# Optimization experiments

Hardware: AMD Instinct MI355X
Metric: run time of the kernel (lower is better)

The kernel has to match this reference:

```python
import jax, jax.numpy as jnp
import numpy as np

B, S, D, H = 2, 2048, 2048, 16
DH = D // H  # 128


def setup_inputs() -> dict:
    key = jax.random.key(0)
    ks = jax.random.split(key, 7)
    x = jax.random.normal(ks[0], (B, S, D), dtype=jnp.float32)
    # causal mask [b, s, s], True = attend
    mask = jnp.broadcast_to(jnp.tril(jnp.ones((S, S), dtype=bool)), (B, S, S))
    scale = 1.0 / np.sqrt(D)
    Wq = jax.random.normal(ks[1], (D, H, DH), dtype=jnp.float32) * scale
    Wk = jax.random.normal(ks[2], (D, 1, DH), dtype=jnp.float32) * scale
    Wv = jax.random.normal(ks[3], (D, 1, DH), dtype=jnp.float32) * scale
    Wo = jax.random.normal(ks[4], (H, DH, D), dtype=jnp.float32) * scale
    bo = jnp.zeros((D,), dtype=jnp.float32)
    return {"x": x, "mask": mask, "Wq": Wq, "Wk": Wk, "Wv": Wv, "Wo": Wo, "bo": bo}


def reference(x, mask, Wq, Wk, Wv, Wo, bo):
    # projections: q [b,s,h,dh]; k,v [b,s,1,dh] (single shared KV head)
    q = jnp.einsum("bsd,dhe->bshe", x, Wq)
    k = jnp.einsum("bsd,dhe->bshe", x, Wk)[:, :, 0, :]  # [b,s,dh]
    v = jnp.einsum("bsd,dhe->bshe", x, Wv)[:, :, 0, :]  # [b,s,dh]
    # scores [b,h,s,s] with 1/sqrt(d_head) scaling
    scores = jnp.einsum("bqhe,bke->bhqk", q, k) / jnp.sqrt(
        jnp.asarray(q.shape[-1], dtype=q.dtype)
    )
    big_neg = jnp.finfo(scores.dtype).min
    scores = jnp.where(mask[:, None, :, :], scores, big_neg)
    probs = jax.nn.softmax(scores, axis=-1)
    attn = jnp.einsum("bhqk,bke->bhqe", probs, v)  # [b,h,s,dh]
    # output projection contracting (head, d_head) -> d_state, with bias
    out = jnp.einsum("bhqe,hed->bqd", attn, Wo) + bo
    return out
```

## Files before the change

kernel.cpp:

```cpp
#include <hip/hip_runtime.h>
#include <cmath>
#include <cstdint>

typedef __bf16 bf16;
typedef __bf16 bf16x8 __attribute__((ext_vector_type(8)));
typedef __bf16 bf16x4 __attribute__((ext_vector_type(4)));
typedef float f32x4 __attribute__((ext_vector_type(4)));

#define SDIM 2048
#define DDIM 2048
#define NQKV 2304
#define DH   128

__device__ __forceinline__ void glds16(const bf16* g, bf16* l) {
    __builtin_amdgcn_global_load_lds(
        (const __attribute__((address_space(1))) void*)g,
        (__attribute__((address_space(3))) void*)l, 16, 0, 0);
}

#define MEMFENCE() asm volatile("" ::: "memory")
#define SBAR() do { MEMFENCE(); __builtin_amdgcn_s_barrier(); MEMFENCE(); } while (0)

__global__ __launch_bounds__(256) void prep_kernel(const float* __restrict__ x,
                                                   const float* __restrict__ Wq,
                                                   const float* __restrict__ Wk,
                                                   const float* __restrict__ Wv,
                                                   const float* __restrict__ Wo,
                                                   bf16* __restrict__ xb,
                                                   bf16* __restrict__ Wqkv_t,
                                                   bf16* __restrict__ Wo_t) {
    __shared__ float tile[32][33];
    int bx = blockIdx.x;
    if (bx < 8192) {
        int i = bx * 256 + threadIdx.x;
        float4 v = reinterpret_cast<const float4*>(x)[i];
        bf16x4 o;
        o[0] = (bf16)v.x; o[1] = (bf16)v.y; o[2] = (bf16)v.z; o[3] = (bf16)v.w;
        reinterpret_cast<bf16x4*>(xb)[i] = o;
        return;
    }
    bx -= 8192;
    const float* src; bf16* dst; int srcN; int t;
    if (bx < 4096)      { src = Wq; dst = Wqkv_t;                      srcN = 2048; t = bx; }
    else if (bx < 4352) { src = Wk; dst = Wqkv_t + (size_t)2048*2048;  srcN = 128;  t = bx - 4096; }
    else if (bx < 4608) { src = Wv; dst = Wqkv_t + (size_t)2176*2048;  srcN = 128;  t = bx - 4352; }
    else                { src = Wo; dst = Wo_t;                        srcN = 2048; t = bx - 4608; }
    const int srcK = 2048;
    int ntx = srcN >> 5;
    int n0 = (t % ntx) * 32, k0 = (t / ntx) * 32;
    int tx = threadIdx.x & 31;
    int ty = threadIdx.x >> 5;
    for (int i = 0; i < 4; i++)
        tile[ty + i*8][tx] = src[(size_t)(k0 + ty + i*8) * srcN + n0 + tx];
    __syncthreads();
    for (int i = 0; i < 4; i++)
        dst[(size_t)(n0 + ty + i*8) * srcK + k0 + tx] = (bf16)tile[tx][ty + i*8];
}

template<int WRITE_F32, int BNW, int WRITE_VT>
__global__ __launch_bounds__(512, 2) void gemm9_kernel(const bf16* __restrict__ A,
                                                       const bf16* __restrict__ Bt,
                                                       void* __restrict__ Cout,
                                                       const float* __restrict__ bias,
                                                       bf16* __restrict__ Vt,
                                                       int N) {
    constexpr int K    = 2048;
    constexpr int NT   = 64;
    constexpr int ABUF = 8192;
    constexpr int BBUF = BNW * 2048;
    constexpr int GPT  = 2 + (BNW >> 1);
    __shared__ bf16 smem[3 * ABUF + 3 * BBUF];

    const int tid  = threadIdx.x;
    const int wave = tid >> 6, lane = tid & 63;
    const int quad = lane >> 4, l15 = lane & 15;
    const int wm = wave >> 2, wn = wave & 3;
    const int tm = blockIdx.x * 256, tn = blockIdx.y * (64 * BNW);

    const int rr = wave * 16 + (lane >> 2);
    const int cs = (lane & 3) ^ ((lane >> 3) & 3);
    const bf16* Ag = A  + (size_t)(tm + rr) * K + cs * 8;
    const bf16* Bg = Bt + (size_t)(tn + rr) * K + cs * 8;
    bf16* Asl = smem + wave * 512;
    bf16* Bsl = smem + 3 * ABUF + wave * 512;

    auto STAGE = [&](int t, int s3) {
        const bf16* sa = Ag + t * 32;
        bf16* da = Asl + s3 * ABUF;
        glds16(sa, da);
        glds16(sa + 128 * K, da + 4096);
        const bf16* sb = Bg + t * 32;
        bf16* db = Bsl + s3 * BBUF;
        glds16(sb, db);
        if constexpr (BNW == 4) glds16(sb + 128 * K, db + 4096);
    };

    const int rsw  = (l15 >> 1) & 3;
    const int coff = (quad ^ rsw) * 8;

    f32x4 acc[8][BNW];
#pragma unroll
    for (int m = 0; m < 8; m++)
#pragma unroll
        for (int n = 0; n < BNW; n++) acc[m][n] = (f32x4)0.0f;

    STAGE(0, 0);
    STAGE(1, 1);
    if constexpr (BNW == 4) asm volatile("s_waitcnt vmcnt(4)" ::: "memory");
    else                    asm volatile("s_waitcnt vmcnt(3)" ::: "memory");
    SBAR();

    int b3 = 0, s3 = 2;
    for (int t = 0; t < NT; ++t) {
        if (t + 2 < NT) STAGE(t + 2, s3);

        const bf16* Ab = smem + b3 * ABUF;
        const bf16* Bb = smem + 3 * ABUF + b3 * BBUF;
        bf16x8 av[8], bv[BNW];
#pragma unroll
        for (int m = 0; m < 8; m++)
            av[m] = *reinterpret_cast<const bf16x8*>(Ab + (wm*128 + m*16 + l15) * 32 + coff);
#pragma unroll
        for (int n = 0; n < BNW; n++)
            bv[n] = *reinterpret_cast<const bf16x8*>(Bb + (wn*16*BNW + n*16 + l15) * 32 + coff);

        __builtin_amdgcn_s_setprio(1);
#pragma unroll
        for (int m = 0; m < 8; m++)
#pragma unroll
            for (int n = 0; n < BNW; n++)
                acc[m][n] = __builtin_amdgcn_mfma_f32_16x16x32_bf16(av[m], bv[n], acc[m][n], 0, 0, 0);
        __builtin_amdgcn_s_setprio(0);

        if (t + 2 < NT) {
            if constexpr (BNW == 4) asm volatile("s_waitcnt vmcnt(4)" ::: "memory");
            else                    asm volatile("s_waitcnt vmcnt(3)" ::: "memory");
        } else {
            asm volatile("s_waitcnt vmcnt(0)" ::: "memory");
        }
        SBAR();
        b3 = (b3 == 2) ? 0 : b3 + 1;
        s3 = (s3 == 2) ? 0 : s3 + 1;
    }

#pragma unroll
    for (int m = 0; m < 8; m++)
#pragma unroll
        for (int n = 0; n < BNW; n++) {
#pragma unroll
            for (int r = 0; r < 4; r++) {
                int row = tm + wm * 128 + m * 16 + quad * 4 + r;
                int col = tn + wn * 16 * BNW + n * 16 + l15;
                float v = acc[m][n][r];
                if (WRITE_F32)
                    reinterpret_cast<float*>(Cout)[(size_t)row * N + col] = v + bias[col];
                else
                    reinterpret_cast<bf16*>(Cout)[(size_t)row * N + col] = (bf16)v;
            }
            if constexpr (WRITE_VT) {
                if (tn == 2048 && wn >= 2) {
                    int col  = tn + wn * 16 * BNW + n * 16 + l15;
                    int d    = col - 2176;
                    int row0 = tm + wm * 128 + m * 16 + quad * 4;
                    int bb   = row0 >> 11;
                    int s0v  = row0 & 2047;
                    int pp0  = (s0v & ~63) | (s0v & 32) | ((s0v & 12) << 1) | ((s0v & 16) >> 2);
                    bf16x4 vv;
                    vv[0] = (bf16)acc[m][n][0]; vv[1] = (bf16)acc[m][n][1];
                    vv[2] = (bf16)acc[m][n][2]; vv[3] = (bf16)acc[m][n][3];
                    *reinterpret_cast<bf16x4*>(Vt + ((size_t)bb * DH + d) * SDIM + pp0) = vv;
                }
            }
        }
}

__global__ __launch_bounds__(512, 4) void flash_kernel(const bf16* __restrict__ QKV,
                                                       const bf16* __restrict__ Vt,
                                                       bf16* __restrict__ attn) {
    __shared__ __align__(16) bf16 KVS[32768];
    const int tid  = threadIdx.x;
    const int wave = tid >> 6, lane = tid & 63;
    const int quad = lane >> 4, l15 = lane & 15;
    const int bx = blockIdx.x;
    const int u  = (bx < 256) ? bx : bx - 256;
    const int qs = (bx < 256) ? (255 - (u >> 1)) : (u >> 1);
    const int b  = u & 1;
    const int q  = qs * 8 + wave;
    const size_t rowbase = (size_t)b * SDIM;
    const bf16* Vtb = Vt + (size_t)b * DH * SDIM;
    const float scale = 0.088388347648318447f;

    const int s0 = wave, s1 = wave + 8;
    const int krow0 = s0*4 + quad, krow1 = s1*4 + quad;
    const bf16* kp0 = QKV + (rowbase + krow0) * NQKV + 2048 + ((l15 ^ (krow0 & 15)) * 8);
    const bf16* kp1 = QKV + (rowbase + krow1) * NQKV + 2048 + ((l15 ^ (krow1 & 15)) * 8);
    const int vrow0 = s0*8 + (lane >> 3), vrow1 = s1*8 + (lane >> 3);
    const bf16* vp0 = Vtb + (size_t)vrow0 * SDIM + (((lane & 7) ^ (vrow0 & 7)) * 8);
    const bf16* vp1 = Vtb + (size_t)vrow1 * SDIM + (((lane & 7) ^ (vrow1 & 7)) * 8);

    bf16x8 qf[4];
    {
        const bf16* qp = QKV + (rowbase + q) * NQKV + l15 * DH + quad * 8;
#pragma unroll
        for (int kk = 0; kk < 4; kk++) qf[kk] = *reinterpret_cast<const bf16x8*>(qp + kk * 32);
    }

    f32x4 acc[8];
#pragma unroll
    for (int d = 0; d < 8; d++) acc[d] = (f32x4)0.0f;
    float l_s = 0.0f;

    const int ntiles = (qs >> 3) + 1;

    glds16(kp0, KVS + s0 * 512);         glds16(kp1, KVS + s1 * 512);
    glds16(vp0, KVS + 16384 + s0 * 512); glds16(vp1, KVS + 16384 + s1 * 512);
    kp0 += 64 * NQKV; kp1 += 64 * NQKV; vp0 += 64; vp1 += 64;

    for (int t = 0; t < ntiles; t++) {
        asm volatile("s_waitcnt vmcnt(2)" ::: "memory");
        SBAR();
        if (t + 1 < ntiles) {
            bf16* kb = KVS + ((t + 1) & 1) * 8192;
            glds16(kp0, kb + s0 * 512); glds16(kp1, kb + s1 * 512);
            kp0 += 64 * NQKV; kp1 += 64 * NQKV;
        }
        const bf16* Ks  = KVS + (t & 1) * 8192;
        const bf16* Vts = KVS + 16384 + (t & 1) * 8192;
        const int key0 = t * 64;

        f32x4 sc[4];
#pragma unroll
        for (int c = 0; c < 4; c++) sc[c] = (f32x4)0.0f;
        __builtin_amdgcn_s_setprio(1);
#pragma unroll
        for (int c = 0; c < 4; c++)
#pragma unroll
            for (int kk = 0; kk < 4; kk++) {
                bf16x8 kf = *reinterpret_cast<const bf16x8*>(
                    Ks + (c*16 + l15) * 128 + (((kk*4 + quad) ^ l15) * 8));
                sc[c] = __builtin_amdgcn_mfma_f32_16x16x32_bf16(kf, qf[kk], sc[c], 0, 0, 0);
            }
        __builtin_amdgcn_s_setprio(0);

        bf16x8 pa[2];
        {
            const bool tail = (key0 + 63 > q);
            float ps = 0.0f;
#pragma unroll
            for (int c = 0; c < 4; c++)
#pragma unroll
                for (int r = 0; r < 4; r++) {
                    int key = key0 + c*16 + quad*4 + r;
                    float pv = (tail && key > q) ? 0.0f : __expf(sc[c][r] * scale);
                    ps += pv;
                    pa[c >> 1][(c & 1)*4 + r] = (bf16)pv;
                }
            l_s += ps;
        }

        if (t + 1 < ntiles) asm volatile("s_waitcnt vmcnt(2)" ::: "memory");
        else                asm volatile("s_waitcnt vmcnt(0)" ::: "memory");

        __builtin_amdgcn_s_setprio(1);
#pragma unroll
        for (int kk2 = 0; kk2 < 2; kk2++)
#pragma unroll
            for (int dd = 0; dd < 8; dd++) {
                bf16x8 vf = *reinterpret_cast<const bf16x8*>(
                    Vts + (dd*16 + l15) * 64 + (((kk2*4 + quad) ^ (l15 & 7)) * 8));
                acc[dd] = __builtin_amdgcn_mfma_f32_16x16x32_bf16(pa[kk2], vf, acc[dd], 0, 0, 0);
            }
        __builtin_amdgcn_s_setprio(0);

        if (t + 1 < ntiles) {
            bf16* vb = KVS + 16384 + ((t + 1) & 1) * 8192;
            glds16(vp0, vb + s0 * 512); glds16(vp1, vb + s1 * 512);
            vp0 += 64; vp1 += 64;
        }
    }

    __syncthreads();

    float linv;
    {
        float v = l_s;
        v += __shfl_xor(v, 16);
        v += __shfl_xor(v, 32);
        linv = 1.0f / v;
    }

    bf16* Ow = KVS + wave * 2048;
#pragma unroll
    for (int r = 0; r < 4; r++) {
        float inv = __shfl(linv, quad*4 + r);
#pragma unroll
        for (int dd = 0; dd < 8; dd++)
            Ow[(quad*4 + r)*128 + dd*16 + l15] = (bf16)(acc[dd][r] * inv);
    }
    const int orow = lane >> 2;
    const int ocol = (lane & 3) * 8;
    bf16* ob = attn + (rowbase + q) * (size_t)DDIM;
#pragma unroll
    for (int it = 0; it < 4; it++)
        *reinterpret_cast<uint4*>(ob + orow * DH + ocol + it*32) =
            *reinterpret_cast<const uint4*>(Ow + orow * 128 + ocol + it*32);
}

extern "C" void kernel_launch(void* const* d_in, const int* in_sizes, int n_in,
                              void* d_out, int out_size, void* d_ws, size_t ws_size,
                              hipStream_t stream) {
    const float* x  = (const float*)d_in[0];
    const float* Wq = (const float*)d_in[2];
    const float* Wk = (const float*)d_in[3];
    const float* Wv = (const float*)d_in[4];
    const float* Wo = (const float*)d_in[5];
    const float* bo = (const float*)d_in[6];
    float* out = (float*)d_out;

    char* ws = (char*)d_ws;
    bf16* xb     = (bf16*)(ws);
    bf16* Wqkv_t = (bf16*)(ws + 16777216);
    bf16* Wo_t   = (bf16*)(ws + 26214400);
    bf16* QKV    = (bf16*)(ws + 34603008);
    bf16* attn   = (bf16*)(ws + 53477376);
    bf16* Vtb    = (bf16*)(ws + 70254592);
    (void)ws_size; (void)in_sizes; (void)n_in; (void)out_size;

    prep_kernel<<<16896, 256, 0, stream>>>(x, Wq, Wk, Wv, Wo, xb, Wqkv_t, Wo_t);
    gemm9_kernel<0, 4, 1><<<dim3(16, 9), 512, 0, stream>>>(xb, Wqkv_t, (void*)QKV, nullptr, Vtb, 2304);
    flash_kernel<<<512, 512, 0, stream>>>(QKV, Vtb, attn);
    gemm9_kernel<1, 2, 0><<<dim3(16, 16), 512, 0, stream>>>(attn, Wo_t, (void*)out, bo, nullptr, 2048);
}
```

Before: 280.9 us.

## Switch GEMM to BK=64 double-buffered tiles and retile QKV GEMM to BN=192

The GEMM is rewritten with a 64-wide K step and two LDS buffers instead of a 32-wide K step with a triple-buffered pipeline. This halves the number of barriers and loop iterations, and the new XOR swizzle spans 8 chunks. The QKV projection now uses 192-wide N tiles over 12 column blocks, giving 192 blocks instead of 144 for better CU coverage on 256 CUs. In exchange, each iteration waits with vmcnt(0) before its barrier, so prefetch only runs one stage ahead and less load latency is hidden.

```diff
diff --git a/kernel.cpp b/kernel.cpp
--- a/kernel.cpp
+++ b/kernel.cpp
@@ -58,18 +58,18 @@
 }
 
 template<int WRITE_F32, int BNW, int WRITE_VT>
-__global__ __launch_bounds__(512, 2) void gemm9_kernel(const bf16* __restrict__ A,
-                                                       const bf16* __restrict__ Bt,
-                                                       void* __restrict__ Cout,
-                                                       const float* __restrict__ bias,
-                                                       bf16* __restrict__ Vt,
-                                                       int N) {
-    constexpr int K    = 2048;
-    constexpr int NT   = 64;
-    constexpr int ABUF = 8192;
-    constexpr int BBUF = BNW * 2048;
-    constexpr int GPT  = 2 + (BNW >> 1);
-    __shared__ bf16 smem[3 * ABUF + 3 * BBUF];
+__global__ __launch_bounds__(512, 2) void gemm10_kernel(const bf16* __restrict__ A,
+                                                        const bf16* __restrict__ Bt,
+                                                        void* __restrict__ Cout,
+                                                        const float* __restrict__ bias,
+                                                        bf16* __restrict__ Vt,
+                                                        int N) {
+    constexpr int K     = 2048;
+    constexpr int NT    = 32;
+    constexpr int ABUF  = 16384;
+    constexpr int BBUF  = BNW * 4096;
+    constexpr int BUFSZ = ABUF + BBUF;
+    __shared__ bf16 smem[2 * BUFSZ];
 
     const int tid  = threadIdx.x;
     const int wave = tid >> 6, lane = tid & 63;
@@ -77,27 +77,22 @@
     const int wm = wave >> 2, wn = wave & 3;
     const int tm = blockIdx.x * 256, tn = blockIdx.y * (64 * BNW);
 
-    const int rr = wave * 16 + (lane >> 2);
-    const int cs = (lane & 3) ^ ((lane >> 3) & 3);
-    const bf16* Ag = A  + (size_t)(tm + rr) * K + cs * 8;
-    const bf16* Bg = Bt + (size_t)(tn + rr) * K + cs * 8;
-    bf16* Asl = smem + wave * 512;
-    bf16* Bsl = smem + 3 * ABUF + wave * 512;
-
-    auto STAGE = [&](int t, int s3) {
-        const bf16* sa = Ag + t * 32;
-        bf16* da = Asl + s3 * ABUF;
-        glds16(sa, da);
-        glds16(sa + 128 * K, da + 4096);
-        const bf16* sb = Bg + t * 32;
-        bf16* db = Bsl + s3 * BBUF;
-        glds16(sb, db);
-        if constexpr (BNW == 4) glds16(sb + 128 * K, db + 4096);
+    const int rowi = lane >> 3;
+    const int cs8  = (lane & 7) ^ rowi;
+    const bf16* Ag = A  + (size_t)(tm + wave * 8 + rowi) * K + cs8 * 8;
+    const bf16* Bg = Bt + (size_t)(tn + wave * 8 + rowi) * K + cs8 * 8;
+
+    auto STAGE = [&](int t, int bb) {
+        const bf16* sa = Ag + t * 64;
+        bf16* da = smem + bb * BUFSZ + wave * 512;
+#pragma unroll
+        for (int p = 0; p < 4; p++) glds16(sa + (size_t)p * 64 * K, da + p * 4096);
+        const bf16* sb = Bg + t * 64;
+        bf16* db = smem + bb * BUFSZ + ABUF + wave * 512;
+#pragma unroll
+        for (int p = 0; p < BNW; p++) glds16(sb + (size_t)p * 64 * K, db + p * 4096);
     };
 
-    const int rsw  = (l15 >> 1) & 3;
-    const int coff = (quad ^ rsw) * 8;
-
     f32x4 acc[8][BNW];
 #pragma unroll
     for (int m = 0; m < 8; m++)
@@ -105,52 +100,47 @@
         for (int n = 0; n < BNW; n++) acc[m][n] = (f32x4)0.0f;
 
     STAGE(0, 0);
-    STAGE(1, 1);
-    if constexpr (BNW == 4) asm volatile("s_waitcnt vmcnt(4)" ::: "memory");
-    else                    asm volatile("s_waitcnt vmcnt(3)" ::: "memory");
+    asm volatile("s_waitcnt vmcnt(0)" ::: "memory");
     SBAR();
 
-    int b3 = 0, s3 = 2;
     for (int t = 0; t < NT; ++t) {
-        if (t + 2 < NT) STAGE(t + 2, s3);
-
-        const bf16* Ab = smem + b3 * ABUF;
-        const bf16* Bb = smem + 3 * ABUF + b3 * BBUF;
-        bf16x8 av[8], bv[BNW];
-#pragma unroll
-        for (int m = 0; m < 8; m++)
-            av[m] = *reinterpret_cast<const bf16x8*>(Ab + (wm*128 + m*16 + l15) * 32 + coff);
-#pragma unroll
-        for (int n = 0; n < BNW; n++)
-            bv[n] = *reinterpret_cast<const bf16x8*>(Bb + (wn*16*BNW + n*16 + l15) * 32 + coff);
-
-        __builtin_amdgcn_s_setprio(1);
-#pragma unroll
-        for (int m = 0; m < 8; m++)
+        if (t + 1 < NT) STAGE(t + 1, (t + 1) & 1);
+
+        const bf16* Ab = smem + (t & 1) * BUFSZ;
+        const bf16* Bb = Ab + ABUF;
+#pragma unroll
+        for (int kh = 0; kh < 2; kh++) {
+            bf16x8 av[8], bv[BNW];
+#pragma unroll
+            for (int m = 0; m < 8; m++)
+                av[m] = *reinterpret_cast<const bf16x8*>(
+                    Ab + (wm*128 + m*16 + l15) * 64 + (((kh*4 + quad) ^ (l15 & 7)) * 8));
 #pragma unroll
             for (int n = 0; n < BNW; n++)
-                acc[m][n] = __builtin_amdgcn_mfma_f32_16x16x32_bf16(av[m], bv[n], acc[m][n], 0, 0, 0);
-        __builtin_amdgcn_s_setprio(0);
-
-        if (t + 2 < NT) {
-            if constexpr (BNW == 4) asm volatile("s_waitcnt vmcnt(4)" ::: "memory");
-            else                    asm volatile("s_waitcnt vmcnt(3)" ::: "memory");
-        } else {
-            asm volatile("s_waitcnt vmcnt(0)" ::: "memory");
-        }
+                bv[n] = *reinterpret_cast<const bf16x8*>(
+                    Bb + (wn*16*BNW + n*16 + l15) * 64 + (((kh*4 + quad) ^ (l15 & 7)) * 8));
+
+            __builtin_amdgcn_s_setprio(1);
+#pragma unroll
+            for (int m = 0; m < 8; m++)
+#pragma unroll
+                for (int n = 0; n < BNW; n++)
+                    acc[m][n] = __builtin_amdgcn_mfma_f32_16x16x32_bf16(av[m], bv[n], acc[m][n], 0, 0, 0);
+            __builtin_amdgcn_s_setprio(0);
+        }
+
+        asm volatile("s_waitcnt vmcnt(0)" ::: "memory");
         SBAR();
-        b3 = (b3 == 2) ? 0 : b3 + 1;
-        s3 = (s3 == 2) ? 0 : s3 + 1;
     }
 
 #pragma unroll
     for (int m = 0; m < 8; m++)
 #pragma unroll
         for (int n = 0; n < BNW; n++) {
+            int col = tn + wn * 16 * BNW + n * 16 + l15;
 #pragma unroll
             for (int r = 0; r < 4; r++) {
                 int row = tm + wm * 128 + m * 16 + quad * 4 + r;
-                int col = tn + wn * 16 * BNW + n * 16 + l15;
                 float v = acc[m][n][r];
                 if (WRITE_F32)
                     reinterpret_cast<float*>(Cout)[(size_t)row * N + col] = v + bias[col];
@@ -158,8 +148,7 @@
                     reinterpret_cast<bf16*>(Cout)[(size_t)row * N + col] = (bf16)v;
             }
             if constexpr (WRITE_VT) {
-                if (tn == 2048 && wn >= 2) {
-                    int col  = tn + wn * 16 * BNW + n * 16 + l15;
+                if (col >= 2176) {
                     int d    = col - 2176;
                     int row0 = tm + wm * 128 + m * 16 + quad * 4;
                     int bb   = row0 >> 11;
@@ -327,7 +316,7 @@
     (void)ws_size; (void)in_sizes; (void)n_in; (void)out_size;
 
     prep_kernel<<<16896, 256, 0, stream>>>(x, Wq, Wk, Wv, Wo, xb, Wqkv_t, Wo_t);
-    gemm9_kernel<0, 4, 1><<<dim3(16, 9), 512, 0, stream>>>(xb, Wqkv_t, (void*)QKV, nullptr, Vtb, 2304);
+    gemm10_kernel<0, 3, 1><<<dim3(16, 12), 512, 0, stream>>>(xb, Wqkv_t, (void*)QKV, nullptr, Vtb, 2304);
     flash_kernel<<<512, 512, 0, stream>>>(QKV, Vtb, attn);
-    gemm9_kernel<1, 2, 0><<<dim3(16, 16), 512, 0, stream>>>(attn, Wo_t, (void*)out, bo, nullptr, 2048);
-}
+    gemm10_kernel<1, 2, 0><<<dim3(16, 16), 512, 0, stream>>>(attn, Wo_t, (void*)out, bo, nullptr, 2048);
+}
```

Result: faster. 266.8 us (-5.0%).
